# Kernel optimization log

Hardware: AMD Instinct MI355X
Metric: run time of the kernel (lower is better)

## Reference

```python
import jax, jax.numpy as jnp
import numpy as np

ROUTINGS = 3

def squash(v):
    # v: [..., D]
    n = jnp.linalg.norm(v, axis=-1, keepdims=True)
    n2 = n * n
    return (n2 / (1.0 + n2)) * v / (n + 1e-8)

def setup_inputs() -> dict:
    key = jax.random.key(0)
    k1, k2 = jax.random.split(key)
    B, O, I, D_out, D_in = 64, 32, 512, 64, 64
    x = jax.random.normal(k1, (B, I, D_in), dtype=jnp.float32)
    # xavier_uniform with gain=1.141 over last two dims (out_dim, in_dim)
    fan_in, fan_out = D_in, D_out
    bound = 1.141 * np.sqrt(6.0 / (fan_in + fan_out))
    weight = jax.random.uniform(k2, (O, I, D_out, D_in), dtype=jnp.float32,
                                minval=-bound, maxval=bound)
    return {"x": x, "weight": weight}

def reference(x, weight):
    # x: [B, I, D_in]; weight: [O, I, D_out, D_in]
    B = x.shape[0]
    O, I = weight.shape[0], weight.shape[1]
    # x_hat[b,o,i,d] = sum_m W[o,i,d,m] x[b,i,m]  -> [B, O, I, D_out]
    x_hat = jnp.einsum('oidm,bim->boid', weight, x)
    x_hat_detach = jax.lax.stop_gradient(x_hat)
    b = jnp.zeros((B, O, I), dtype=x.dtype)
    out = None
    for i in range(ROUTINGS):
        c = jax.nn.softmax(b, axis=1)  # softmax over out_num
        if i == ROUTINGS - 1:
            out = squash(jnp.einsum('boi,boid->bod', c, x_hat))
        else:
            out = squash(jnp.einsum('boi,boid->bod', c, x_hat_detach))
            # agreement: [B,O,I,D] . [B,O,D] -> [B,O,I]
            b = b + jnp.einsum('boid,bod->boi', x_hat_detach, out)
    return out  # [B, O, D_out]
```

## Files before the change

### kernel.cpp

```cpp
#include <hip/hip_runtime.h>
#include <stdint.h>

#define NB 64
#define NO 32
#define NI 512
#define ND 64

typedef __attribute__((ext_vector_type(8))) short short8;
typedef __attribute__((ext_vector_type(4))) float f32x4;

#define GL2LDS(g, s) __builtin_amdgcn_global_load_lds( \
    (const __attribute__((address_space(1))) void*)(g), \
    (__attribute__((address_space(3))) void*)(s), 16, 0, 0)

__device__ __forceinline__ float blo(unsigned int u) {
    union { unsigned int i; float f; } v; v.i = u << 16; return v.f;
}
__device__ __forceinline__ float bhi(unsigned int u) {
    union { unsigned int i; float f; } v; v.i = u & 0xFFFF0000u; return v.f;
}
__device__ __forceinline__ unsigned short f2bf(float f) {
    union { float f; unsigned int i; } v; v.f = f;
    return (unsigned short)((v.i + 0x7FFFu + ((v.i >> 16) & 1u)) >> 16);
}
__device__ __forceinline__ short8 pack8(const float4 a, const float4 b) {
    short8 r;
    r[0] = (short)f2bf(a.x); r[1] = (short)f2bf(a.y);
    r[2] = (short)f2bf(a.z); r[3] = (short)f2bf(a.w);
    r[4] = (short)f2bf(b.x); r[5] = (short)f2bf(b.y);
    r[6] = (short)f2bf(b.z); r[7] = (short)f2bf(b.w);
    return r;
}
__device__ __forceinline__ void ld_a(float4 r[4], const float* __restrict__ p) {
    r[0] = *(const float4*)(p);
    r[1] = *(const float4*)(p + 4);
    r[2] = *(const float4*)(p + 32);
    r[3] = *(const float4*)(p + 36);
}

__global__ __launch_bounds__(256) void k_gemm(const float* __restrict__ x,
                                              const float* __restrict__ w,
                                              unsigned short* __restrict__ xh) {
    __shared__ float Wl[3][4096];
    const int o  = blockIdx.x & 31;
    const int ig = blockIdx.x >> 5;
    const int t  = threadIdx.x;
    const int wv = t >> 6;
    const int l  = t & 63;
    const int q  = l >> 4;
    const int c  = l & 15;

    const float* wbase = w + ((size_t)o * NI + ig * 8) * 4096;

    auto stage = [&](int buf, int ii) {
        const float* src = wbase + (size_t)ii * 4096;
        #pragma unroll
        for (int k = 0; k < 4; ++k) {
            const int s = wv * 256 + k * 64 + l;
            const int r = s >> 4;
            const int g = (s & 15) ^ (r & 15);
            GL2LDS(src + r * 64 + g * 4, &Wl[buf][(wv * 256 + k * 64) * 4]);
        }
    };

    const float* ap0 = x + ((size_t)(16 * wv + c) * NI + ig * 8) * 64 + q * 8;
    float4 ra[4], na[4];
    ld_a(ra, ap0);
    stage(0, 0);
    stage(1, 1);

    #pragma unroll
    for (int ii = 0; ii < 8; ++ii) {
        __syncthreads();
        if (ii < 6) stage((ii + 2) % 3, ii + 2);
        if (ii < 7) ld_a(na, ap0 + (ii + 1) * 64);

        const int i = ig * 8 + ii;
        const float* Wb = Wl[ii % 3];
        const short8 a0 = pack8(ra[0], ra[1]);
        const short8 a1 = pack8(ra[2], ra[3]);
        f32x4 acc[4];
        #pragma unroll
        for (int td = 0; td < 4; ++td) {
            const int r = 16 * td + c;
            const float4 f0 = *(const float4*)&Wb[(r * 16 + ((2 * q)     ^ c)) * 4];
            const float4 f1 = *(const float4*)&Wb[(r * 16 + ((2 * q + 1) ^ c)) * 4];
            const float4 f2 = *(const float4*)&Wb[(r * 16 + ((2 * q + 8) ^ c)) * 4];
            const float4 f3 = *(const float4*)&Wb[(r * 16 + ((2 * q + 9) ^ c)) * 4];
            const short8 b0 = pack8(f0, f1);
            const short8 b1 = pack8(f2, f3);
            f32x4 z = {0.f, 0.f, 0.f, 0.f};
            z = __builtin_amdgcn_mfma_f32_16x16x32_bf16(a0, b0, z, 0, 0, 0);
            z = __builtin_amdgcn_mfma_f32_16x16x32_bf16(a1, b1, z, 0, 0, 0);
            acc[td] = z;
        }
        #pragma unroll
        for (int td = 0; td < 4; ++td) {
            const int d = 16 * td + c;
            #pragma unroll
            for (int rr = 0; rr < 4; ++rr) {
                const int b = 16 * wv + 4 * q + rr;
                xh[(((size_t)o * NB + b) * NI + i) * ND + d] = f2bf(acc[td][rr]);
            }
        }
        #pragma unroll
        for (int j = 0; j < 4; ++j) ra[j] = na[j];
    }
}

__global__ __launch_bounds__(256) void k_soft(const float* __restrict__ b_in,
                                              float* __restrict__ mz) {
    const int p = blockIdx.x * 256 + threadIdx.x;
    const int b = p >> 9, i = p & 511;
    const float* bp = b_in + (size_t)b * NO * NI + i;
    float v[NO];
    #pragma unroll
    for (int oo = 0; oo < NO; ++oo) v[oo] = bp[(size_t)oo * NI];
    float m = v[0];
    #pragma unroll
    for (int oo = 1; oo < NO; ++oo) m = fmaxf(m, v[oo]);
    float Z = 0.f;
    #pragma unroll
    for (int oo = 0; oo < NO; ++oo) Z += __expf(v[oo] - m);
    mz[p] = m;
    mz[NB * NI + p] = 1.0f / Z;
}

template<int STEP>
__global__ __launch_bounds__(256) void k_route(const unsigned short* __restrict__ xh,
                                               const float* __restrict__ b_in,
                                               const float* __restrict__ mz,
                                               float* __restrict__ b_out,
                                               float* __restrict__ outp) {
    extern __shared__ char smem[];
    unsigned short* tile = (unsigned short*)smem;
    __shared__ float c_s[NI];
    __shared__ float P[4 * 64];
    __shared__ float o_s[64];

    const int t  = threadIdx.x;
    const int b  = blockIdx.x >> 5;
    const int o  = blockIdx.x & 31;
    const int wv = t >> 6;
    const int l  = t & 63;
    const int dg = t & 7;
    const int ip = t >> 3;

    const unsigned short* gsrc = xh + ((size_t)o * NB + b) * NI * ND;
    #pragma unroll
    for (int k = 0; k < 16; ++k) {
        GL2LDS(gsrc + wv * 8192 + k * 512 + l * 8, tile + wv * 8192 + k * 512);
    }

    const float* bp = (STEP > 0) ? (b_in + ((size_t)b * NO + o) * NI) : nullptr;
    if (STEP > 0) {
        const float* mrow = mz + (size_t)b * NI;
        const float* zrow = mz + (size_t)(NB * NI) + (size_t)b * NI;
        #pragma unroll
        for (int s = 0; s < 2; ++s) {
            const int i = t + s * 256;
            c_s[i] = __expf(bp[i] - mrow[i]) * zrow[i];
        }
    }
    __syncthreads();

    float acc[8] = {0, 0, 0, 0, 0, 0, 0, 0};
    #pragma unroll
    for (int k = 0; k < 16; ++k) {
        const int i = 32 * k + ip;
        const uint4 raw = *(const uint4*)(tile + i * ND + dg * 8);
        const float cw = (STEP == 0) ? 0.03125f : c_s[i];
        acc[0] += cw * blo(raw.x); acc[1] += cw * bhi(raw.x);
        acc[2] += cw * blo(raw.y); acc[3] += cw * bhi(raw.y);
        acc[4] += cw * blo(raw.z); acc[5] += cw * bhi(raw.z);
        acc[6] += cw * blo(raw.w); acc[7] += cw * bhi(raw.w);
    }
    #pragma unroll
    for (int j = 0; j < 8; ++j) {
        acc[j] += __shfl_xor(acc[j], 8);
        acc[j] += __shfl_xor(acc[j], 16);
        acc[j] += __shfl_xor(acc[j], 32);
    }
    if (l < 8) {
        #pragma unroll
        for (int j = 0; j < 8; ++j) P[wv * 64 + l * 8 + j] = acc[j];
    }
    __syncthreads();

    if (t < 64) {
        const float sv = P[t] + P[64 + t] + P[128 + t] + P[192 + t];
        float s2 = sv * sv;
        #pragma unroll
        for (int m = 1; m < 64; m <<= 1) s2 += __shfl_xor(s2, m);
        const float n = sqrtf(s2);
        const float sc = (s2 / (1.0f + s2)) / (n + 1e-8f);
        const float ov = sv * sc;
        o_s[t] = ov;
        if (STEP == 2) outp[((size_t)b * NO + o) * ND + t] = ov;
    }
    __syncthreads();

    if (STEP < 2) {
        float oc[8];
        #pragma unroll
        for (int j = 0; j < 8; ++j) oc[j] = o_s[dg * 8 + j];
        float w1 = 0.f, w2 = 0.f;
        #pragma unroll
        for (int k = 0; k < 16; ++k) {
            const uint4 raw = *(const uint4*)(tile + (32 * k + ip) * ND + dg * 8);
            float pd = blo(raw.x) * oc[0] + bhi(raw.x) * oc[1]
                     + blo(raw.y) * oc[2] + bhi(raw.y) * oc[3]
                     + blo(raw.z) * oc[4] + bhi(raw.z) * oc[5]
                     + blo(raw.w) * oc[6] + bhi(raw.w) * oc[7];
            pd += __shfl_xor(pd, 1);
            pd += __shfl_xor(pd, 2);
            pd += __shfl_xor(pd, 4);
            if (k == dg)     w1 = pd;
            if (k == dg + 8) w2 = pd;
        }
        const int i1 = 32 * dg + ip;
        const int i2 = 32 * (dg + 8) + ip;
        float* bo = b_out + ((size_t)b * NO + o) * NI;
        bo[i1] = ((STEP == 0) ? 0.f : bp[i1]) + w1;
        bo[i2] = ((STEP == 0) ? 0.f : bp[i2]) + w2;
    }
}

extern "C" void kernel_launch(void* const* d_in, const int* in_sizes, int n_in,
                              void* d_out, int out_size, void* d_ws, size_t ws_size,
                              hipStream_t stream) {
    const float* x = (const float*)d_in[0];
    const float* w = (const float*)d_in[1];
    float* outp = (float*)d_out;

    char* ws = (char*)d_ws;
    unsigned short* xh = (unsigned short*)ws;
    float* ba = (float*)(ws + (size_t)134217728);
    float* bb = (float*)(ws + (size_t)134217728 + 4194304);
    float* mz = (float*)(ws + (size_t)134217728 + 2 * 4194304);

    const int smem = 65536;
    hipFuncSetAttribute(reinterpret_cast<const void*>(&k_route<0>),
                        hipFuncAttributeMaxDynamicSharedMemorySize, smem);
    hipFuncSetAttribute(reinterpret_cast<const void*>(&k_route<1>),
                        hipFuncAttributeMaxDynamicSharedMemorySize, smem);
    hipFuncSetAttribute(reinterpret_cast<const void*>(&k_route<2>),
                        hipFuncAttributeMaxDynamicSharedMemorySize, smem);

    k_gemm<<<dim3(2048), dim3(256), 0, stream>>>(x, w, xh);
    k_route<0><<<dim3(2048), dim3(256), smem, stream>>>(xh, nullptr, nullptr, ba, nullptr);
    k_soft<<<dim3(128), dim3(256), 0, stream>>>(ba, mz);
    k_route<1><<<dim3(2048), dim3(256), smem, stream>>>(xh, ba, mz, bb, nullptr);
    k_soft<<<dim3(128), dim3(256), 0, stream>>>(bb, mz);
    k_route<2><<<dim3(2048), dim3(256), smem, stream>>>(xh, bb, mz, nullptr, outp);
}
```

Measured before the change: 487.0 us.

## Pack bf16 x_hat stores and halve routing LDS tile by holding half in registers

The GEMM kernel now packs four bf16 outputs into one 8-byte store per row and defers each iteration's stores to the next loop iteration, so they overlap with the MFMA work. The intended cost removed is many scattered 2-byte global writes. This permutes the d ordering within xh (4*c+td instead of 16*td+c), and the routing kernel compensates when it writes the final output. The routing kernel stages only half of each x_hat row in LDS (32KB, static) and keeps the other half in registers via direct global loads, which should allow more blocks per CU at the cost of higher register pressure.

```diff
diff --git a/kernel.cpp b/kernel.cpp
--- a/kernel.cpp
+++ b/kernel.cpp
@@ -69,13 +69,20 @@
     stage(0, 0);
     stage(1, 1);
 
+    uint2 cst[4];
     #pragma unroll
     for (int ii = 0; ii < 8; ++ii) {
         __syncthreads();
+        if (ii > 0) {
+            #pragma unroll
+            for (int rr = 0; rr < 4; ++rr) {
+                const int bq = 16 * wv + 4 * q + rr;
+                *(uint2*)(xh + (((size_t)o * NB + bq) * NI + (ig * 8 + ii - 1)) * ND + 4 * c) = cst[rr];
+            }
+        }
         if (ii < 6) stage((ii + 2) % 3, ii + 2);
         if (ii < 7) ld_a(na, ap0 + (ii + 1) * 64);
 
-        const int i = ig * 8 + ii;
         const float* Wb = Wl[ii % 3];
         const short8 a0 = pack8(ra[0], ra[1]);
         const short8 a1 = pack8(ra[2], ra[3]);
@@ -95,16 +102,17 @@
             acc[td] = z;
         }
         #pragma unroll
-        for (int td = 0; td < 4; ++td) {
-            const int d = 16 * td + c;
-            #pragma unroll
-            for (int rr = 0; rr < 4; ++rr) {
-                const int b = 16 * wv + 4 * q + rr;
-                xh[(((size_t)o * NB + b) * NI + i) * ND + d] = f2bf(acc[td][rr]);
-            }
+        for (int rr = 0; rr < 4; ++rr) {
+            cst[rr].x = (unsigned int)f2bf(acc[0][rr]) | ((unsigned int)f2bf(acc[1][rr]) << 16);
+            cst[rr].y = (unsigned int)f2bf(acc[2][rr]) | ((unsigned int)f2bf(acc[3][rr]) << 16);
         }
         #pragma unroll
         for (int j = 0; j < 4; ++j) ra[j] = na[j];
+    }
+    #pragma unroll
+    for (int rr = 0; rr < 4; ++rr) {
+        const int bq = 16 * wv + 4 * q + rr;
+        *(uint2*)(xh + (((size_t)o * NB + bq) * NI + (ig * 8 + 7)) * ND + 4 * c) = cst[rr];
     }
 }
 
@@ -132,8 +140,7 @@
                                                const float* __restrict__ mz,
                                                float* __restrict__ b_out,
                                                float* __restrict__ outp) {
-    extern __shared__ char smem[];
-    unsigned short* tile = (unsigned short*)smem;
+    __shared__ unsigned short tile[256 * ND];
     __shared__ float c_s[NI];
     __shared__ float P[4 * 64];
     __shared__ float o_s[64];
@@ -147,10 +154,15 @@
     const int ip = t >> 3;
 
     const unsigned short* gsrc = xh + ((size_t)o * NB + b) * NI * ND;
-    #pragma unroll
-    for (int k = 0; k < 16; ++k) {
-        GL2LDS(gsrc + wv * 8192 + k * 512 + l * 8, tile + wv * 8192 + k * 512);
-    }
+
+    uint4 raw[8];
+    #pragma unroll
+    for (int k = 0; k < 8; ++k)
+        raw[k] = *(const uint4*)(gsrc + (size_t)(256 + 32 * k + ip) * ND + dg * 8);
+
+    #pragma unroll
+    for (int k = 0; k < 8; ++k)
+        GL2LDS(gsrc + wv * 4096 + k * 512 + l * 8, tile + wv * 4096 + k * 512);
 
     const float* bp = (STEP > 0) ? (b_in + ((size_t)b * NO + o) * NI) : nullptr;
     if (STEP > 0) {
@@ -166,14 +178,22 @@
 
     float acc[8] = {0, 0, 0, 0, 0, 0, 0, 0};
     #pragma unroll
-    for (int k = 0; k < 16; ++k) {
+    for (int k = 0; k < 8; ++k) {
         const int i = 32 * k + ip;
-        const uint4 raw = *(const uint4*)(tile + i * ND + dg * 8);
+        const uint4 rl = *(const uint4*)(tile + i * ND + dg * 8);
         const float cw = (STEP == 0) ? 0.03125f : c_s[i];
-        acc[0] += cw * blo(raw.x); acc[1] += cw * bhi(raw.x);
-        acc[2] += cw * blo(raw.y); acc[3] += cw * bhi(raw.y);
-        acc[4] += cw * blo(raw.z); acc[5] += cw * bhi(raw.z);
-        acc[6] += cw * blo(raw.w); acc[7] += cw * bhi(raw.w);
+        acc[0] += cw * blo(rl.x); acc[1] += cw * bhi(rl.x);
+        acc[2] += cw * blo(rl.y); acc[3] += cw * bhi(rl.y);
+        acc[4] += cw * blo(rl.z); acc[5] += cw * bhi(rl.z);
+        acc[6] += cw * blo(rl.w); acc[7] += cw * bhi(rl.w);
+    }
+    #pragma unroll
+    for (int k = 0; k < 8; ++k) {
+        const float cw = (STEP == 0) ? 0.03125f : c_s[256 + 32 * k + ip];
+        acc[0] += cw * blo(raw[k].x); acc[1] += cw * bhi(raw[k].x);
+        acc[2] += cw * blo(raw[k].y); acc[3] += cw * bhi(raw[k].y);
+        acc[4] += cw * blo(raw[k].z); acc[5] += cw * bhi(raw[k].z);
+        acc[6] += cw * blo(raw[k].w); acc[7] += cw * bhi(raw[k].w);
     }
     #pragma unroll
     for (int j = 0; j < 8; ++j) {
@@ -196,7 +216,10 @@
         const float sc = (s2 / (1.0f + s2)) / (n + 1e-8f);
         const float ov = sv * sc;
         o_s[t] = ov;
-        if (STEP == 2) outp[((size_t)b * NO + o) * ND + t] = ov;
+        if (STEP == 2) {
+            const int d = 16 * (t & 3) + (t >> 2);
+            outp[((size_t)b * NO + o) * ND + d] = ov;
+        }
     }
     __syncthreads();
 
@@ -206,20 +229,30 @@
         for (int j = 0; j < 8; ++j) oc[j] = o_s[dg * 8 + j];
         float w1 = 0.f, w2 = 0.f;
         #pragma unroll
-        for (int k = 0; k < 16; ++k) {
-            const uint4 raw = *(const uint4*)(tile + (32 * k + ip) * ND + dg * 8);
-            float pd = blo(raw.x) * oc[0] + bhi(raw.x) * oc[1]
-                     + blo(raw.y) * oc[2] + bhi(raw.y) * oc[3]
-                     + blo(raw.z) * oc[4] + bhi(raw.z) * oc[5]
-                     + blo(raw.w) * oc[6] + bhi(raw.w) * oc[7];
+        for (int k = 0; k < 8; ++k) {
+            const uint4 rl = *(const uint4*)(tile + (32 * k + ip) * ND + dg * 8);
+            float pd = blo(rl.x) * oc[0] + bhi(rl.x) * oc[1]
+                     + blo(rl.y) * oc[2] + bhi(rl.y) * oc[3]
+                     + blo(rl.z) * oc[4] + bhi(rl.z) * oc[5]
+                     + blo(rl.w) * oc[6] + bhi(rl.w) * oc[7];
             pd += __shfl_xor(pd, 1);
             pd += __shfl_xor(pd, 2);
             pd += __shfl_xor(pd, 4);
-            if (k == dg)     w1 = pd;
-            if (k == dg + 8) w2 = pd;
+            if (k == dg) w1 = pd;
+        }
+        #pragma unroll
+        for (int k = 0; k < 8; ++k) {
+            float pd = blo(raw[k].x) * oc[0] + bhi(raw[k].x) * oc[1]
+                     + blo(raw[k].y) * oc[2] + bhi(raw[k].y) * oc[3]
+                     + blo(raw[k].z) * oc[4] + bhi(raw[k].z) * oc[5]
+                     + blo(raw[k].w) * oc[6] + bhi(raw[k].w) * oc[7];
+            pd += __shfl_xor(pd, 1);
+            pd += __shfl_xor(pd, 2);
+            pd += __shfl_xor(pd, 4);
+            if (k == dg) w2 = pd;
         }
         const int i1 = 32 * dg + ip;
-        const int i2 = 32 * (dg + 8) + ip;
+        const int i2 = 256 + 32 * dg + ip;
         float* bo = b_out + ((size_t)b * NO + o) * NI;
         bo[i1] = ((STEP == 0) ? 0.f : bp[i1]) + w1;
         bo[i2] = ((STEP == 0) ? 0.f : bp[i2]) + w2;
@@ -239,18 +272,10 @@
     float* bb = (float*)(ws + (size_t)134217728 + 4194304);
     float* mz = (float*)(ws + (size_t)134217728 + 2 * 4194304);
 
-    const int smem = 65536;
-    hipFuncSetAttribute(reinterpret_cast<const void*>(&k_route<0>),
-                        hipFuncAttributeMaxDynamicSharedMemorySize, smem);
-    hipFuncSetAttribute(reinterpret_cast<const void*>(&k_route<1>),
-                        hipFuncAttributeMaxDynamicSharedMemorySize, smem);
-    hipFuncSetAttribute(reinterpret_cast<const void*>(&k_route<2>),
-                        hipFuncAttributeMaxDynamicSharedMemorySize, smem);
-
     k_gemm<<<dim3(2048), dim3(256), 0, stream>>>(x, w, xh);
-    k_route<0><<<dim3(2048), dim3(256), smem, stream>>>(xh, nullptr, nullptr, ba, nullptr);
+    k_route<0><<<dim3(2048), dim3(256), 0, stream>>>(xh, nullptr, nullptr, ba, nullptr);
     k_soft<<<dim3(128), dim3(256), 0, stream>>>(ba, mz);
-    k_route<1><<<dim3(2048), dim3(256), smem, stream>>>(xh, ba, mz, bb, nullptr);
+    k_route<1><<<dim3(2048), dim3(256), 0, stream>>>(xh, ba, mz, bb, nullptr);
     k_soft<<<dim3(128), dim3(256), 0, stream>>>(bb, mz);
-    k_route<2><<<dim3(2048), dim3(256), smem, stream>>>(xh, bb, mz, nullptr, outp);
-}
+    k_route<2><<<dim3(2048), dim3(256), 0, stream>>>(xh, bb, mz, nullptr, outp);
+}
```

Result: faster. 466.1 us (-4.3%).
